# Kernel optimization log

Hardware: AMD Instinct MI355X
Metric: run time of the kernel (lower is better)

The kernel has to match this reference:

```python
import jax, jax.numpy as jnp
import numpy as np

N = 100000
E = 3200000
G = 64  # number of graphs


def _lin_params(key, fan_in, fan_out):
    k1, k2 = jax.random.split(key)
    bound = 1.0 / np.sqrt(fan_in)
    W = jax.random.uniform(k1, (fan_in, fan_out), jnp.float32, -bound, bound)
    b = jax.random.uniform(k2, (fan_out,), jnp.float32, -bound, bound)
    return W, b


def setup_inputs() -> dict:
    key = jax.random.key(0)
    ks = jax.random.split(key, 12)
    x = jax.random.normal(ks[0], (N, 3), jnp.float32)
    edge_index = jax.random.randint(ks[1], (2, E), 0, N, jnp.int32)
    batch = jnp.sort(jax.random.randint(ks[2], (N,), 0, G, jnp.int32))
    # conv1: in=3, heads=4, out_channels=16, concat=True -> 64
    Wq1, bq1 = _lin_params(ks[3], 3, 64)
    Wk1, bk1 = _lin_params(ks[4], 3, 64)
    Wv1, bv1 = _lin_params(ks[5], 3, 64)
    Ws1, bs1 = _lin_params(ks[6], 3, 64)
    # conv2: in=64, heads=1, out_channels=6, concat=False -> 6
    Wq2, bq2 = _lin_params(ks[7], 64, 6)
    Wk2, bk2 = _lin_params(ks[8], 64, 6)
    Wv2, bv2 = _lin_params(ks[9], 64, 6)
    Ws2, bs2 = _lin_params(ks[10], 64, 6)
    return dict(x=x, edge_index=edge_index, batch=batch,
                Wq1=Wq1, bq1=bq1, Wk1=Wk1, bk1=bk1, Wv1=Wv1, bv1=bv1, Ws1=Ws1, bs1=bs1,
                Wq2=Wq2, bq2=bq2, Wk2=Wk2, bk2=bk2, Wv2=Wv2, bv2=bv2, Ws2=Ws2, bs2=bs2)


def transformer_conv(x, src, dst, Wq, bq, Wk, bk, Wv, bv, Ws, bs, heads, d, concat):
    n = x.shape[0]
    q = (x @ Wq + bq).reshape(n, heads, d)
    k = (x @ Wk + bk).reshape(n, heads, d)
    v = (x @ Wv + bv).reshape(n, heads, d)
    # per-edge attention logits: query at target, key at source  [E, H]
    logits = jnp.einsum('ehd,ehd->eh', q[dst], k[src]) / jnp.sqrt(jnp.float32(d))
    # segment softmax over incoming edges of each target node
    m = jax.ops.segment_max(logits, dst, num_segments=n)          # [N, H]
    a = jnp.exp(logits - m[dst])                                   # [E, H]
    denom = jax.ops.segment_sum(a, dst, num_segments=n)           # [N, H]
    alpha = a / (denom[dst] + 1e-16)
    out = jax.ops.segment_sum(alpha[:, :, None] * v[src], dst, num_segments=n)  # [N,H,d]
    out = out.reshape(n, heads * d) if concat else out.mean(axis=1)
    return out + x @ Ws + bs  # root/skip connection


def reference(x, edge_index, batch,
              Wq1, bq1, Wk1, bk1, Wv1, bv1, Ws1, bs1,
              Wq2, bq2, Wk2, bk2, Wv2, bv2, Ws2, bs2):
    src, dst = edge_index[0], edge_index[1]
    h = transformer_conv(x, src, dst, Wq1, bq1, Wk1, bk1, Wv1, bv1, Ws1, bs1,
                         heads=4, d=16, concat=True)
    h = jax.nn.relu(h)
    # dropout is identity in eval mode
    h = transformer_conv(h, src, dst, Wq2, bq2, Wk2, bk2, Wv2, bv2, Ws2, bs2,
                         heads=1, d=6, concat=False)
    # global mean pool over graphs
    sums = jax.ops.segment_sum(h, batch, num_segments=G)
    cnts = jax.ops.segment_sum(jnp.ones((h.shape[0],), h.dtype), batch, num_segments=G)
    pooled = sums / jnp.maximum(cnts, 1.0)[:, None]
    return jax.nn.log_softmax(pooled, axis=1)
```

## Files before the change

### kernel.cpp

```cpp
#include <hip/hip_runtime.h>
#include <hip/hip_fp16.h>
#include <math.h>

#define N_NODES 100000
#define N_EDGES 3200000
#define N_GRAPHS 64
#define NEG_INF -1e30f

#define NB 196
#define CAP 18432
#define NBLK 512
#define CHUNK 6250

__device__ __forceinline__ void atomAddF(float* p, float v) {
#if defined(__HIP_PLATFORM_AMD__)
    unsafeAtomicAdd(p, v);
#else
    atomicAdd(p, v);
#endif
}

__device__ __forceinline__ float b2f(unsigned w, int sh) {
    return (float)(signed char)(w >> sh);
}

__device__ __forceinline__ float kvdot(const float* q, uint4 w, float* sv_out) {
    float2 s = __half22float2(*(const __half2*)&w.w);
    *sv_out = s.y;
    return s.x * (q[0] * b2f(w.x, 0) + q[1] * b2f(w.x, 8)
                + q[2] * b2f(w.x, 16) + q[3] * b2f(w.x, 24)
                + q[4] * b2f(w.y, 0) + q[5] * b2f(w.y, 8));
}

__global__ void k0_packx(const float* __restrict__ x, float4* __restrict__ xp,
                         uint2* __restrict__ xh) {
    int n = blockIdx.x * 256 + threadIdx.x;
    if (n >= N_NODES) return;
    float x0 = x[3 * n], x1 = x[3 * n + 1], x2 = x[3 * n + 2];
    xp[n] = make_float4(x0, x1, x2, 0.f);
    __half2 h01 = __floats2half2_rn(x0, x1);
    __half2 h2p = __floats2half2_rn(x2, 0.f);
    xh[n] = make_uint2(*(unsigned*)&h01, *(unsigned*)&h2p);
}

__global__ __launch_bounds__(512) void s1_partition(const int* __restrict__ ei,
                                                    int* __restrict__ offs,
                                                    unsigned* __restrict__ pairs) {
    __shared__ unsigned pairbuf[CHUNK];
    __shared__ unsigned sortbuf[CHUNK];
    __shared__ unsigned char buckbuf[CHUNK];
    __shared__ int hist[4][200];
    __shared__ int cur[NB], tmp[NB];
    int tid = threadIdx.x;
    int wp = tid >> 7;
    for (int i = tid; i < 4 * 200; i += 512) ((int*)hist)[i] = 0;
    __syncthreads();
    int gbase = blockIdx.x * CHUNK;
    for (int i = tid; i < CHUNK; i += 512) {
        int src = ei[gbase + i];
        unsigned dst = (unsigned)ei[N_EDGES + gbase + i];
        pairbuf[i] = ((unsigned)src << 9) | (dst & 511u);
        unsigned b = dst >> 9;
        buckbuf[i] = (unsigned char)b;
        atomicAdd(&hist[wp][b], 1);
    }
    __syncthreads();
    if (tid < NB)
        tmp[tid] = hist[0][tid] + hist[1][tid] + hist[2][tid] + hist[3][tid];
    __syncthreads();
    for (int off = 1; off < NB; off <<= 1) {
        int v = 0;
        if (tid < NB && tid >= off) v = tmp[tid - off];
        __syncthreads();
        if (tid < NB) tmp[tid] += v;
        __syncthreads();
    }
    if (tid < NB) {
        int cnt_b = hist[0][tid] + hist[1][tid] + hist[2][tid] + hist[3][tid];
        int excl = tmp[tid] - cnt_b;
        cur[tid] = excl;
        offs[blockIdx.x * NB + tid] = excl;
    }
    __syncthreads();
    for (int i = tid; i < CHUNK; i += 512) {
        int pos = atomicAdd(&cur[buckbuf[i]], 1);
        sortbuf[pos] = pairbuf[i];
    }
    __syncthreads();
    for (int i = tid; i < CHUNK; i += 512)
        pairs[gbase + i] = sortbuf[i];
}

#define B4T 1024
__global__ __launch_bounds__(B4T) void b4_build(const unsigned* __restrict__ pairs,
                                                const int* __restrict__ offs,
                                                int* __restrict__ rs,
                                                int* __restrict__ re,
                                                int* __restrict__ csr_src) {
    __shared__ unsigned eLDS[CAP];
    __shared__ int so[NBLK], slen[NBLK], dbase[NBLK];
    __shared__ int cnt[512], sc[512], cur[512];
    int b = blockIdx.x;
    int tid = threadIdx.x;

    for (int k = tid; k < NBLK; k += B4T) {
        int s = offs[k * NB + b];
        int e = (b == NB - 1) ? CHUNK : offs[k * NB + b + 1];
        so[k] = s;
        slen[k] = e - s;
    }
    __syncthreads();
    if (tid < NBLK) sc[tid] = slen[tid];
    __syncthreads();
    for (int off = 1; off < NBLK; off <<= 1) {
        int v = (tid < NBLK && tid >= off) ? sc[tid - off] : 0;
        __syncthreads();
        if (tid < NBLK) sc[tid] += v;
        __syncthreads();
    }
    if (tid < NBLK) dbase[tid] = sc[tid] - slen[tid];
    __syncthreads();
    int ne = dbase[NBLK - 1] + slen[NBLK - 1];

    int wave = tid >> 6, lane = tid & 63;
    for (int k = wave; k < NBLK; k += (B4T / 64)) {
        int gb = k * CHUNK + so[k];
        int db = dbase[k], ln = slen[k];
        for (int i = lane; i < ln; i += 64)
            eLDS[db + i] = pairs[gb + i];
    }
    if (tid < 512) cnt[tid] = 0;
    __syncthreads();

    for (int i = tid; i < ne; i += B4T)
        atomicAdd(&cnt[eLDS[i] & 511u], 1);
    __syncthreads();
    if (tid < 512) sc[tid] = cnt[tid];
    __syncthreads();
    for (int off = 1; off < 512; off <<= 1) {
        int v = (tid < 512 && tid >= off) ? sc[tid - off] : 0;
        __syncthreads();
        if (tid < 512) sc[tid] += v;
        __syncthreads();
    }
    int rbase = b * CAP;
    if (tid < 512) {
        int excl = sc[tid] - cnt[tid];
        cur[tid] = rbase + excl;
        int node = (b << 9) + tid;
        if (node < N_NODES) {
            rs[node] = rbase + excl;
            re[node] = rbase + sc[tid];
        }
    }
    __syncthreads();
    for (int i = tid; i < ne; i += B4T) {
        unsigned p = eLDS[i];
        int pos = atomicAdd(&cur[p & 511u], 1);
        csr_src[pos] = (int)(p >> 9);
    }
}

__global__ void g1_layer1(const float4* __restrict__ xp,
                          const uint2* __restrict__ xh,
                          const float* __restrict__ Wq, const float* __restrict__ bq,
                          const float* __restrict__ Wk, const float* __restrict__ bk,
                          const float* __restrict__ Wv, const float* __restrict__ bv,
                          const float* __restrict__ Ws, const float* __restrict__ bs,
                          const int* __restrict__ rs, const int* __restrict__ re,
                          const int* __restrict__ csr_src,
                          uint2* __restrict__ h1) {
    __shared__ float sWq[192], sWk[192], sWv[192], sWs[192];
    __shared__ float sbq[64], sbk[64], sbv[64], sbs[64];
    for (int i = threadIdx.x; i < 192; i += 256) {
        sWq[i] = Wq[i]; sWk[i] = Wk[i]; sWv[i] = Wv[i]; sWs[i] = Ws[i];
    }
    for (int i = threadIdx.x; i < 64; i += 256) {
        sbq[i] = bq[i]; sbk[i] = bk[i]; sbv[i] = bv[i]; sbs[i] = bs[i];
    }
    __syncthreads();

    int lane = threadIdx.x & 63;
    int u = lane & 15;
    int slot = u >> 2;
    int j0 = u * 4;
    int n = blockIdx.x * 16 + (threadIdx.x >> 6) * 4 + (lane >> 4);

    float4 xc = xp[n];
    float x0 = xc.x, x1 = xc.y, x2 = xc.z;

    float q[4];
#pragma unroll
    for (int i = 0; i < 4; ++i)
        q[i] = 0.25f * (sbq[j0 + i] + x0 * sWq[j0 + i] + x1 * sWq[64 + j0 + i]
                        + x2 * sWq[128 + j0 + i]);
    float t0 = 0.f, t1 = 0.f, t2 = 0.f, tb = 0.f;
#pragma unroll
    for (int i = 0; i < 4; ++i) {
        float qi = q[i];
        t0 += qi * sWk[j0 + i];
        t1 += qi * sWk[64 + j0 + i];
        t2 += qi * sWk[128 + j0 + i];
        tb += qi * sbk[j0 + i];
    }
#pragma unroll
    for (int off = 1; off <= 2; off <<= 1) {
        t0 += __shfl_xor(t0, off);
        t1 += __shfl_xor(t1, off);
        t2 += __shfl_xor(t2, off);
        tb += __shfl_xor(tb, off);
    }
    int tsrc = (lane & 48) | ((lane & 3) << 2) | ((lane >> 2) & 3);
    t0 = __shfl(t0, tsrc, 64);
    t1 = __shfl(t1, tsrc, 64);
    t2 = __shfl(t2, tsrc, 64);
    tb = __shfl(tb, tsrc, 64);

    int row = rs[n];
    int deg = re[n] - row;

    float mA = NEG_INF, dA = 0.f, s0A = 0.f, s1A = 0.f, s2A = 0.f;
    float mB = NEG_INF, dB = 0.f, s0B = 0.f, s1B = 0.f, s2B = 0.f;
    for (int base = 0; base < deg; base += 8) {
        int eA = base + slot, eB = base + 4 + slot;
        bool vA = eA < deg, vB = eB < deg;
        int srcA = vA ? csr_src[row + eA] : 0;
        int srcB = vB ? csr_src[row + eB] : 0;
        uint2 wA = xh[srcA];
        uint2 wB = xh[srcB];
        float2 a01 = __half22float2(*(const __half2*)&wA.x);
        float a2 = __half22float2(*(const __half2*)&wA.y).x;
        float2 b01 = __half22float2(*(const __half2*)&wB.x);
        float b2 = __half22float2(*(const __half2*)&wB.y).x;
        float lA = vA ? (tb + a01.x * t0 + a01.y * t1 + a2 * t2) : NEG_INF;
        float lB = vB ? (tb + b01.x * t0 + b01.y * t1 + b2 * t2) : NEG_INF;
        float mnA = fmaxf(mA, lA);
        float scA = __expf(mA - mnA);
        float aA = vA ? __expf(lA - mnA) : 0.f;
        dA = dA * scA + aA;
        s0A = s0A * scA + aA * a01.x;
        s1A = s1A * scA + aA * a01.y;
        s2A = s2A * scA + aA * a2;
        mA = mnA;
        float mnB = fmaxf(mB, lB);
        float scB = __expf(mB - mnB);
        float aB = vB ? __expf(lB - mnB) : 0.f;
        dB = dB * scB + aB;
        s0B = s0B * scB + aB * b01.x;
        s1B = s1B * scB + aB * b01.y;
        s2B = s2B * scB + aB * b2;
        mB = mnB;
    }
    float m = fmaxf(mA, mB);
    float fA = __expf(mA - m), fB = __expf(mB - m);
    float d = dA * fA + dB * fB;
    float s0 = s0A * fA + s0B * fB;
    float s1 = s1A * fA + s1B * fB;
    float s2 = s2A * fA + s2B * fB;

    float gm = m;
    gm = fmaxf(gm, __shfl_xor(gm, 4));
    gm = fmaxf(gm, __shfl_xor(gm, 8));
    float f = __expf(m - gm);
    d *= f; s0 *= f; s1 *= f; s2 *= f;
#pragma unroll
    for (int off = 4; off <= 8; off <<= 1) {
        d += __shfl_xor(d, off);
        s0 += __shfl_xor(s0, off);
        s1 += __shfl_xor(s1, off);
        s2 += __shfl_xor(s2, off);
    }

    int esrc = (lane & 48) | ((lane >> 2) & 3);
    float dH = __shfl(d, esrc, 64);
    float s0H = __shfl(s0, esrc, 64);
    float s1H = __shfl(s1, esrc, 64);
    float s2H = __shfl(s2, esrc, 64);
    float inv = 1.f / (dH + 1e-16f);
    float fr = dH * inv, r0 = s0H * inv, r1 = s1H * inv, r2 = s2H * inv;

    float o[4];
#pragma unroll
    for (int i = 0; i < 4; ++i) {
        int j = j0 + i;
        float val = fr * sbv[j] + r0 * sWv[j] + r1 * sWv[64 + j] + r2 * sWv[128 + j]
                  + sbs[j] + x0 * sWs[j] + x1 * sWs[64 + j] + x2 * sWs[128 + j];
        o[i] = fmaxf(val, 0.f);
    }
    __half2 p01 = __floats2half2_rn(o[0], o[1]);
    __half2 p23 = __floats2half2_rn(o[2], o[3]);
    h1[(size_t)n * 16 + u] = make_uint2(*(unsigned*)&p01, *(unsigned*)&p23);
}

__global__ void k5_node2(const unsigned* __restrict__ h1,
                         const float* __restrict__ Wq, const float* __restrict__ bq,
                         const float* __restrict__ Wk, const float* __restrict__ bk,
                         const float* __restrict__ Wv, const float* __restrict__ bv,
                         const float* __restrict__ Ws, const float* __restrict__ bs,
                         float* __restrict__ q2, float* __restrict__ s2,
                         uint4* __restrict__ kv2) {
    __shared__ float sWq[384], sWk[384], sWv[384], sWs[384];
    __shared__ float sbq[6], sbk[6], sbv[6], sbs[6];
    for (int i = threadIdx.x; i < 384; i += blockDim.x) {
        sWq[i] = Wq[i]; sWk[i] = Wk[i]; sWv[i] = Wv[i]; sWs[i] = Ws[i];
    }
    if (threadIdx.x < 6) {
        sbq[threadIdx.x] = bq[threadIdx.x];
        sbk[threadIdx.x] = bk[threadIdx.x];
        sbv[threadIdx.x] = bv[threadIdx.x];
        sbs[threadIdx.x] = bs[threadIdx.x];
    }
    __syncthreads();
    int n = blockIdx.x * blockDim.x + threadIdx.x;
    if (n >= N_NODES) return;
    float qa[6], ka[6], va[6], sa[6];
#pragma unroll
    for (int c = 0; c < 6; ++c) { qa[c] = sbq[c]; ka[c] = sbk[c]; va[c] = sbv[c]; sa[c] = sbs[c]; }
    const uint4* hp = reinterpret_cast<const uint4*>(h1 + (size_t)n * 32);
#pragma unroll
    for (int i4 = 0; i4 < 8; ++i4) {
        uint4 hv = hp[i4];
        float2 f01 = __half22float2(*(const __half2*)&hv.x);
        float2 f23 = __half22float2(*(const __half2*)&hv.y);
        float2 f45 = __half22float2(*(const __half2*)&hv.z);
        float2 f67 = __half22float2(*(const __half2*)&hv.w);
        float hvv[8] = {f01.x, f01.y, f23.x, f23.y, f45.x, f45.y, f67.x, f67.y};
#pragma unroll
        for (int uu = 0; uu < 8; ++uu) {
            float hx = hvv[uu];
            int i = i4 * 8 + uu;
#pragma unroll
            for (int c = 0; c < 6; ++c) {
                qa[c] += hx * sWq[i * 6 + c];
                ka[c] += hx * sWk[i * 6 + c];
                va[c] += hx * sWv[i * 6 + c];
                sa[c] += hx * sWs[i * 6 + c];
            }
        }
    }
    const float rsqrt6 = 0.4082482904638631f;
#pragma unroll
    for (int c = 0; c < 6; ++c) {
        q2[(size_t)n * 6 + c] = qa[c] * rsqrt6;
        s2[(size_t)n * 6 + c] = sa[c];
    }
    float mk = 0.f, mv = 0.f;
#pragma unroll
    for (int c = 0; c < 6; ++c) {
        mk = fmaxf(mk, fabsf(ka[c]));
        mv = fmaxf(mv, fabsf(va[c]));
    }
    float sk = fmaxf(mk, 1e-8f) * (1.f / 127.f);
    float sv = fmaxf(mv, 1e-8f) * (1.f / 127.f);
    float isk = 1.f / sk, isv = 1.f / sv;
    int qk[6], qv[6];
#pragma unroll
    for (int c = 0; c < 6; ++c) {
        qk[c] = __float2int_rn(ka[c] * isk);
        qv[c] = __float2int_rn(va[c] * isv);
    }
    uint4 w;
    w.x = (qk[0] & 255) | ((qk[1] & 255) << 8) | ((qk[2] & 255) << 16) | ((qk[3] & 255) << 24);
    w.y = (qk[4] & 255) | ((qk[5] & 255) << 8) | ((qv[0] & 255) << 16) | ((qv[1] & 255) << 24);
    w.z = (qv[2] & 255) | ((qv[3] & 255) << 8) | ((qv[4] & 255) << 16) | ((qv[5] & 255) << 24);
    __half2 hs = __floats2half2_rn(sk, sv);
    w.w = *(unsigned*)&hs;
    kv2[n] = w;
}

__global__ void g2_layer2(const int* __restrict__ rs, const int* __restrict__ re,
                          const int* __restrict__ csr_src,
                          const float* __restrict__ q2,
                          const uint4* __restrict__ kv2,
                          const float* __restrict__ s2,
                          const int* __restrict__ batch,
                          float* __restrict__ psum, float* __restrict__ pcnt) {
    __shared__ float bsum[N_GRAPHS * 6];
    __shared__ float bcnt[N_GRAPHS];
    for (int i = threadIdx.x; i < N_GRAPHS * 6; i += 256) bsum[i] = 0.f;
    for (int i = threadIdx.x; i < N_GRAPHS; i += 256) bcnt[i] = 0.f;
    __syncthreads();

    int node = blockIdx.x * 32 + (threadIdx.x >> 3);
    int lane8 = threadIdx.x & 7;

    float q[6];
#pragma unroll
    for (int c = 0; c < 6; ++c) q[c] = q2[(size_t)node * 6 + c];
    int row = rs[node];
    int deg = re[node] - row;

    float lg[8], svr[8];
    unsigned py[8], pz[8];
#pragma unroll
    for (int i = 0; i < 8; ++i) { lg[i] = NEG_INF; svr[i] = 0.f; py[i] = 0u; pz[i] = 0u; }
    float lmax = NEG_INF;
#pragma unroll
    for (int i = 0; i < 4; ++i) {
        int e = lane8 + i * 8;
        bool v = e < deg;
        int src = v ? csr_src[row + e] : 0;
        uint4 w = kv2[src];
        float svx;
        float l = kvdot(q, w, &svx);
        if (v) {
            lg[i] = l; svr[i] = svx; py[i] = w.y; pz[i] = w.z;
            lmax = fmaxf(lmax, l);
        }
    }
    if (deg > 32) {
#pragma unroll
        for (int i = 4; i < 8; ++i) {
            int e = lane8 + i * 8;
            bool v = e < deg;
            int src = v ? csr_src[row + e] : 0;
            uint4 w = kv2[src];
            float svx;
            float l = kvdot(q, w, &svx);
            if (v) {
                lg[i] = l; svr[i] = svx; py[i] = w.y; pz[i] = w.z;
                lmax = fmaxf(lmax, l);
            }
        }
    }
    float mo = NEG_INF, dov = 0.f;
    float ao[6] = {0.f, 0.f, 0.f, 0.f, 0.f, 0.f};
    for (int e = lane8 + 64; e < deg; e += 8) {
        int src = csr_src[row + e];
        uint4 w = kv2[src];
        float svx;
        float l = kvdot(q, w, &svx);
        float mn = fmaxf(mo, l);
        float scp = __expf(mo - mn);
        float wx = __expf(l - mn);
        float wsx = wx * svx;
        dov = dov * scp + wx;
        ao[0] = ao[0] * scp + wsx * b2f(w.y, 16);
        ao[1] = ao[1] * scp + wsx * b2f(w.y, 24);
        ao[2] = ao[2] * scp + wsx * b2f(w.z, 0);
        ao[3] = ao[3] * scp + wsx * b2f(w.z, 8);
        ao[4] = ao[4] * scp + wsx * b2f(w.z, 16);
        ao[5] = ao[5] * scp + wsx * b2f(w.z, 24);
        mo = mn;
    }
    lmax = fmaxf(lmax, mo);
    lmax = fmaxf(lmax, __shfl_xor(lmax, 1));
    lmax = fmaxf(lmax, __shfl_xor(lmax, 2));
    lmax = fmaxf(lmax, __shfl_xor(lmax, 4));
    if (lmax < -5e29f) lmax = 0.f;

    float d = 0.f;
    float acc[6] = {0.f, 0.f, 0.f, 0.f, 0.f, 0.f};
#pragma unroll
    for (int i = 0; i < 8; ++i) {
        float w = __expf(lg[i] - lmax);
        float ws = w * svr[i];
        d += w;
        acc[0] += ws * b2f(py[i], 16);
        acc[1] += ws * b2f(py[i], 24);
        acc[2] += ws * b2f(pz[i], 0);
        acc[3] += ws * b2f(pz[i], 8);
        acc[4] += ws * b2f(pz[i], 16);
        acc[5] += ws * b2f(pz[i], 24);
    }
    float so = __expf(mo - lmax);
    d += dov * so;
#pragma unroll
    for (int c = 0; c < 6; ++c) acc[c] += ao[c] * so;

#pragma unroll
    for (int off = 1; off <= 4; off <<= 1) {
        d += __shfl_xor(d, off);
#pragma unroll
        for (int c = 0; c < 6; ++c) acc[c] += __shfl_xor(acc[c], off);
    }

    if (lane8 == 0) {
        float inv = 1.f / (d + 1e-16f);
        int g = batch[node];
#pragma unroll
        for (int c = 0; c < 6; ++c) {
            float val = acc[c] * inv + s2[(size_t)node * 6 + c];
            atomicAdd(&bsum[g * 6 + c], val);
        }
        atomicAdd(&bcnt[g], 1.f);
    }
    __syncthreads();
    for (int i = threadIdx.x; i < N_GRAPHS * 6; i += 256) {
        float v = bsum[i];
        if (v != 0.f) atomAddF(psum + i, v);
    }
    for (int i = threadIdx.x; i < N_GRAPHS; i += 256) {
        float v = bcnt[i];
        if (v != 0.f) atomAddF(pcnt + i, v);
    }
}

__global__ void k9_final(const float* __restrict__ psum, const float* __restrict__ pcnt,
                         float* __restrict__ out) {
    int g = threadIdx.x;
    if (g >= N_GRAPHS) return;
    float cnt = fmaxf(pcnt[g], 1.0f);
    float z[6];
    float mx = -1e30f;
#pragma unroll
    for (int c = 0; c < 6; ++c) {
        z[c] = psum[g * 6 + c] / cnt;
        mx = fmaxf(mx, z[c]);
    }
    float se = 0.f;
#pragma unroll
    for (int c = 0; c < 6; ++c) se += __expf(z[c] - mx);
    float lse = mx + logf(se);
#pragma unroll
    for (int c = 0; c < 6; ++c) out[g * 6 + c] = z[c] - lse;
}

extern "C" void kernel_launch(void* const* d_in, const int* in_sizes, int n_in,
                              void* d_out, int out_size, void* d_ws, size_t ws_size,
                              hipStream_t stream) {
    const float* x   = (const float*)d_in[0];
    const int*   ei  = (const int*)d_in[1];
    const int*   bat = (const int*)d_in[2];
    const float* Wq1 = (const float*)d_in[3];  const float* bq1 = (const float*)d_in[4];
    const float* Wk1 = (const float*)d_in[5];  const float* bk1 = (const float*)d_in[6];
    const float* Wv1 = (const float*)d_in[7];  const float* bv1 = (const float*)d_in[8];
    const float* Ws1 = (const float*)d_in[9];  const float* bs1 = (const float*)d_in[10];
    const float* Wq2 = (const float*)d_in[11]; const float* bq2 = (const float*)d_in[12];
    const float* Wk2 = (const float*)d_in[13]; const float* bk2 = (const float*)d_in[14];
    const float* Wv2 = (const float*)d_in[15]; const float* bv2 = (const float*)d_in[16];
    const float* Ws2 = (const float*)d_in[17]; const float* bs2 = (const float*)d_in[18];
    float* out = (float*)d_out;

    char* ws = (char*)d_ws;
    size_t off = 0;
    auto alloc = [&](size_t bytes) -> char* {
        char* p = ws + off;
        off += (bytes + 255) & ~(size_t)255;
        return p;
    };

    float* psum = (float*)alloc((size_t)N_GRAPHS * 6 * 4);
    float* pcnt = (float*)alloc((size_t)N_GRAPHS * 4);
    size_t zero_bytes = off;

    int*      offs    = (int*)     alloc((size_t)NBLK * NB * 4);
    unsigned* pairs   = (unsigned*)alloc((size_t)N_EDGES * 4);
    int*      csr_src = (int*)     alloc((size_t)NB * CAP * 4);
    int*      rsv     = (int*)     alloc((size_t)N_NODES * 4);
    int*      rev     = (int*)     alloc((size_t)N_NODES * 4);
    float4*   xp      = (float4*)  alloc((size_t)N_NODES * 16);
    uint2*    xh      = (uint2*)   alloc((size_t)N_NODES * 8);
    unsigned* h1      = (unsigned*)alloc((size_t)N_NODES * 64 * 2);
    float*    q2      = (float*)   alloc((size_t)N_NODES * 6 * 4);
    float*    s2      = (float*)   alloc((size_t)N_NODES * 6 * 4);
    uint4*    kv2     = (uint4*)   alloc((size_t)N_NODES * 16);

    hipMemsetAsync(d_ws, 0, zero_bytes, stream);

    k0_packx<<<(N_NODES + 255) / 256, 256, 0, stream>>>(x, xp, xh);
    s1_partition<<<NBLK, 512, 0, stream>>>(ei, offs, pairs);
    b4_build<<<NB, B4T, 0, stream>>>(pairs, offs, rsv, rev, csr_src);

    g1_layer1<<<N_NODES / 16, 256, 0, stream>>>(xp, xh, Wq1, bq1, Wk1, bk1, Wv1, bv1,
                                                Ws1, bs1, rsv, rev, csr_src,
                                                (uint2*)h1);
    k5_node2<<<(N_NODES + 255) / 256, 256, 0, stream>>>(h1, Wq2, bq2, Wk2, bk2,
                                                        Wv2, bv2, Ws2, bs2,
                                                        q2, s2, kv2);
    g2_layer2<<<N_NODES / 32, 256, 0, stream>>>(rsv, rev, csr_src, q2, kv2, s2,
                                                bat, psum, pcnt);
    k9_final<<<1, 64, 0, stream>>>(psum, pcnt, out);
}
```

Measured before the change: 144.4 us.

## Fuse layer-2 node projections into layer-1 kernel and spread histogram atomics

Folds the second-layer Q/K/V/skip projections into the layer-1 aggregation kernel. Each lane computes partial dot products over its four output channels and the partials are reduced with cross-lane shuffles. This drops the h1 intermediate buffer (a 12.8MB write plus read) and one kernel launch. The query vector is now stored in fp16, which shrinks the g2 load but adds rounding error. Separately, the partition and CSR-build histograms use more privatised copies to reduce LDS atomic contention. The cost is extra shuffle work and more shared memory in g1.

Result: slower. 158.1 us (+9.5%).

```diff
diff --git a/kernel.cpp b/kernel.cpp
--- a/kernel.cpp
+++ b/kernel.cpp
@@ -49,11 +49,11 @@
     __shared__ unsigned pairbuf[CHUNK];
     __shared__ unsigned sortbuf[CHUNK];
     __shared__ unsigned char buckbuf[CHUNK];
-    __shared__ int hist[4][200];
+    __shared__ int hist[8][200];
     __shared__ int cur[NB], tmp[NB];
     int tid = threadIdx.x;
-    int wp = tid >> 7;
-    for (int i = tid; i < 4 * 200; i += 512) ((int*)hist)[i] = 0;
+    int wp = tid >> 6;
+    for (int i = tid; i < 8 * 200; i += 512) ((int*)hist)[i] = 0;
     __syncthreads();
     int gbase = blockIdx.x * CHUNK;
     for (int i = tid; i < CHUNK; i += 512) {
@@ -65,8 +65,13 @@
         atomicAdd(&hist[wp][b], 1);
     }
     __syncthreads();
-    if (tid < NB)
-        tmp[tid] = hist[0][tid] + hist[1][tid] + hist[2][tid] + hist[3][tid];
+    if (tid < NB) {
+        int s = 0;
+#pragma unroll
+        for (int w = 0; w < 8; ++w) s += hist[w][tid];
+        tmp[tid] = s;
+        hist[0][tid] = s;
+    }
     __syncthreads();
     for (int off = 1; off < NB; off <<= 1) {
         int v = 0;
@@ -76,8 +81,7 @@
         __syncthreads();
     }
     if (tid < NB) {
-        int cnt_b = hist[0][tid] + hist[1][tid] + hist[2][tid] + hist[3][tid];
-        int excl = tmp[tid] - cnt_b;
+        int excl = tmp[tid] - hist[0][tid];
         cur[tid] = excl;
         offs[blockIdx.x * NB + tid] = excl;
     }
@@ -99,7 +103,8 @@
                                                 int* __restrict__ csr_src) {
     __shared__ unsigned eLDS[CAP];
     __shared__ int so[NBLK], slen[NBLK], dbase[NBLK];
-    __shared__ int cnt[512], sc[512], cur[512];
+    __shared__ int cnt2[2][512];
+    __shared__ int sc[512], cur[512];
     int b = blockIdx.x;
     int tid = threadIdx.x;
 
@@ -109,6 +114,7 @@
         so[k] = s;
         slen[k] = e - s;
     }
+    ((int*)cnt2)[tid] = 0;
     __syncthreads();
     if (tid < NBLK) sc[tid] = slen[tid];
     __syncthreads();
@@ -129,13 +135,17 @@
         for (int i = lane; i < ln; i += 64)
             eLDS[db + i] = pairs[gb + i];
     }
-    if (tid < 512) cnt[tid] = 0;
-    __syncthreads();
-
+    __syncthreads();
+
+    int half = tid >> 9;
     for (int i = tid; i < ne; i += B4T)
-        atomicAdd(&cnt[eLDS[i] & 511u], 1);
-    __syncthreads();
-    if (tid < 512) sc[tid] = cnt[tid];
+        atomicAdd(&cnt2[half][eLDS[i] & 511u], 1);
+    __syncthreads();
+    int mycnt = 0;
+    if (tid < 512) {
+        mycnt = cnt2[0][tid] + cnt2[1][tid];
+        sc[tid] = mycnt;
+    }
     __syncthreads();
     for (int off = 1; off < 512; off <<= 1) {
         int v = (tid < 512 && tid >= off) ? sc[tid - off] : 0;
@@ -145,7 +155,7 @@
     }
     int rbase = b * CAP;
     if (tid < 512) {
-        int excl = sc[tid] - cnt[tid];
+        int excl = sc[tid] - mycnt;
         cur[tid] = rbase + excl;
         int node = (b << 9) + tid;
         if (node < N_NODES) {
@@ -161,22 +171,38 @@
     }
 }
 
-__global__ void g1_layer1(const float4* __restrict__ xp,
-                          const uint2* __restrict__ xh,
-                          const float* __restrict__ Wq, const float* __restrict__ bq,
-                          const float* __restrict__ Wk, const float* __restrict__ bk,
-                          const float* __restrict__ Wv, const float* __restrict__ bv,
-                          const float* __restrict__ Ws, const float* __restrict__ bs,
-                          const int* __restrict__ rs, const int* __restrict__ re,
-                          const int* __restrict__ csr_src,
-                          uint2* __restrict__ h1) {
+__global__ void g1_fused(const float4* __restrict__ xp,
+                         const uint2* __restrict__ xh,
+                         const float* __restrict__ Wq, const float* __restrict__ bq,
+                         const float* __restrict__ Wk, const float* __restrict__ bk,
+                         const float* __restrict__ Wv, const float* __restrict__ bv,
+                         const float* __restrict__ Ws, const float* __restrict__ bs,
+                         const float* __restrict__ Wq2, const float* __restrict__ bq2,
+                         const float* __restrict__ Wk2, const float* __restrict__ bk2,
+                         const float* __restrict__ Wv2, const float* __restrict__ bv2,
+                         const float* __restrict__ Ws2, const float* __restrict__ bs2,
+                         const int* __restrict__ rs, const int* __restrict__ re,
+                         const int* __restrict__ csr_src,
+                         uint4* __restrict__ q2h, float* __restrict__ s2,
+                         uint4* __restrict__ kv2) {
     __shared__ float sWq[192], sWk[192], sWv[192], sWs[192];
     __shared__ float sbq[64], sbk[64], sbv[64], sbs[64];
+    __shared__ float sW2q[384], sW2k[384], sW2v[384], sW2s[384];
+    __shared__ float sb2q[6], sb2k[6], sb2v[6], sb2s[6];
     for (int i = threadIdx.x; i < 192; i += 256) {
         sWq[i] = Wq[i]; sWk[i] = Wk[i]; sWv[i] = Wv[i]; sWs[i] = Ws[i];
     }
     for (int i = threadIdx.x; i < 64; i += 256) {
         sbq[i] = bq[i]; sbk[i] = bk[i]; sbv[i] = bv[i]; sbs[i] = bs[i];
+    }
+    for (int i = threadIdx.x; i < 384; i += 256) {
+        sW2q[i] = Wq2[i]; sW2k[i] = Wk2[i]; sW2v[i] = Wv2[i]; sW2s[i] = Ws2[i];
+    }
+    if (threadIdx.x < 6) {
+        sb2q[threadIdx.x] = bq2[threadIdx.x];
+        sb2k[threadIdx.x] = bk2[threadIdx.x];
+        sb2v[threadIdx.x] = bv2[threadIdx.x];
+        sb2s[threadIdx.x] = bs2[threadIdx.x];
     }
     __syncthreads();
 
@@ -256,26 +282,26 @@
     float d = dA * fA + dB * fB;
     float s0 = s0A * fA + s0B * fB;
     float s1 = s1A * fA + s1B * fB;
-    float s2 = s2A * fA + s2B * fB;
+    float s2v = s2A * fA + s2B * fB;
 
     float gm = m;
     gm = fmaxf(gm, __shfl_xor(gm, 4));
     gm = fmaxf(gm, __shfl_xor(gm, 8));
     float f = __expf(m - gm);
-    d *= f; s0 *= f; s1 *= f; s2 *= f;
+    d *= f; s0 *= f; s1 *= f; s2v *= f;
 #pragma unroll
     for (int off = 4; off <= 8; off <<= 1) {
         d += __shfl_xor(d, off);
         s0 += __shfl_xor(s0, off);
         s1 += __shfl_xor(s1, off);
-        s2 += __shfl_xor(s2, off);
+        s2v += __shfl_xor(s2v, off);
     }
 
     int esrc = (lane & 48) | ((lane >> 2) & 3);
     float dH = __shfl(d, esrc, 64);
     float s0H = __shfl(s0, esrc, 64);
     float s1H = __shfl(s1, esrc, 64);
-    float s2H = __shfl(s2, esrc, 64);
+    float s2H = __shfl(s2v, esrc, 64);
     float inv = 1.f / (dH + 1e-16f);
     float fr = dH * inv, r0 = s0H * inv, r1 = s1H * inv, r2 = s2H * inv;
 
@@ -287,90 +313,77 @@
                   + sbs[j] + x0 * sWs[j] + x1 * sWs[64 + j] + x2 * sWs[128 + j];
         o[i] = fmaxf(val, 0.f);
     }
-    __half2 p01 = __floats2half2_rn(o[0], o[1]);
-    __half2 p23 = __floats2half2_rn(o[2], o[3]);
-    h1[(size_t)n * 16 + u] = make_uint2(*(unsigned*)&p01, *(unsigned*)&p23);
-}
-
-__global__ void k5_node2(const unsigned* __restrict__ h1,
-                         const float* __restrict__ Wq, const float* __restrict__ bq,
-                         const float* __restrict__ Wk, const float* __restrict__ bk,
-                         const float* __restrict__ Wv, const float* __restrict__ bv,
-                         const float* __restrict__ Ws, const float* __restrict__ bs,
-                         float* __restrict__ q2, float* __restrict__ s2,
-                         uint4* __restrict__ kv2) {
-    __shared__ float sWq[384], sWk[384], sWv[384], sWs[384];
-    __shared__ float sbq[6], sbk[6], sbv[6], sbs[6];
-    for (int i = threadIdx.x; i < 384; i += blockDim.x) {
-        sWq[i] = Wq[i]; sWk[i] = Wk[i]; sWv[i] = Wv[i]; sWs[i] = Ws[i];
-    }
-    if (threadIdx.x < 6) {
-        sbq[threadIdx.x] = bq[threadIdx.x];
-        sbk[threadIdx.x] = bk[threadIdx.x];
-        sbv[threadIdx.x] = bv[threadIdx.x];
-        sbs[threadIdx.x] = bs[threadIdx.x];
-    }
-    __syncthreads();
-    int n = blockIdx.x * blockDim.x + threadIdx.x;
-    if (n >= N_NODES) return;
-    float qa[6], ka[6], va[6], sa[6];
-#pragma unroll
-    for (int c = 0; c < 6; ++c) { qa[c] = sbq[c]; ka[c] = sbk[c]; va[c] = sbv[c]; sa[c] = sbs[c]; }
-    const uint4* hp = reinterpret_cast<const uint4*>(h1 + (size_t)n * 32);
-#pragma unroll
-    for (int i4 = 0; i4 < 8; ++i4) {
-        uint4 hv = hp[i4];
-        float2 f01 = __half22float2(*(const __half2*)&hv.x);
-        float2 f23 = __half22float2(*(const __half2*)&hv.y);
-        float2 f45 = __half22float2(*(const __half2*)&hv.z);
-        float2 f67 = __half22float2(*(const __half2*)&hv.w);
-        float hvv[8] = {f01.x, f01.y, f23.x, f23.y, f45.x, f45.y, f67.x, f67.y};
-#pragma unroll
-        for (int uu = 0; uu < 8; ++uu) {
-            float hx = hvv[uu];
-            int i = i4 * 8 + uu;
-#pragma unroll
-            for (int c = 0; c < 6; ++c) {
-                qa[c] += hx * sWq[i * 6 + c];
-                ka[c] += hx * sWk[i * 6 + c];
-                va[c] += hx * sWv[i * 6 + c];
-                sa[c] += hx * sWs[i * 6 + c];
-            }
-        }
-    }
+
+    float pq[6], pk[6], pv[6], ps[6];
+#pragma unroll
+    for (int c = 0; c < 6; ++c) { pq[c] = 0.f; pk[c] = 0.f; pv[c] = 0.f; ps[c] = 0.f; }
+#pragma unroll
+    for (int i = 0; i < 4; ++i) {
+        float hx = o[i];
+        int jb = (j0 + i) * 6;
+#pragma unroll
+        for (int c = 0; c < 6; ++c) {
+            pq[c] += hx * sW2q[jb + c];
+            pk[c] += hx * sW2k[jb + c];
+            pv[c] += hx * sW2v[jb + c];
+            ps[c] += hx * sW2s[jb + c];
+        }
+    }
+#pragma unroll
+    for (int off = 1; off <= 8; off <<= 1) {
+#pragma unroll
+        for (int c = 0; c < 6; ++c) {
+            pq[c] += __shfl_xor(pq[c], off);
+            pk[c] += __shfl_xor(pk[c], off);
+            pv[c] += __shfl_xor(pv[c], off);
+            ps[c] += __shfl_xor(ps[c], off);
+        }
+    }
+
     const float rsqrt6 = 0.4082482904638631f;
-#pragma unroll
-    for (int c = 0; c < 6; ++c) {
-        q2[(size_t)n * 6 + c] = qa[c] * rsqrt6;
-        s2[(size_t)n * 6 + c] = sa[c];
-    }
-    float mk = 0.f, mv = 0.f;
-#pragma unroll
-    for (int c = 0; c < 6; ++c) {
-        mk = fmaxf(mk, fabsf(ka[c]));
-        mv = fmaxf(mv, fabsf(va[c]));
-    }
-    float sk = fmaxf(mk, 1e-8f) * (1.f / 127.f);
-    float sv = fmaxf(mv, 1e-8f) * (1.f / 127.f);
-    float isk = 1.f / sk, isv = 1.f / sv;
-    int qk[6], qv[6];
-#pragma unroll
-    for (int c = 0; c < 6; ++c) {
-        qk[c] = __float2int_rn(ka[c] * isk);
-        qv[c] = __float2int_rn(va[c] * isv);
-    }
-    uint4 w;
-    w.x = (qk[0] & 255) | ((qk[1] & 255) << 8) | ((qk[2] & 255) << 16) | ((qk[3] & 255) << 24);
-    w.y = (qk[4] & 255) | ((qk[5] & 255) << 8) | ((qv[0] & 255) << 16) | ((qv[1] & 255) << 24);
-    w.z = (qv[2] & 255) | ((qv[3] & 255) << 8) | ((qv[4] & 255) << 16) | ((qv[5] & 255) << 24);
-    __half2 hs = __floats2half2_rn(sk, sv);
-    w.w = *(unsigned*)&hs;
-    kv2[n] = w;
+    if (u == 0) {
+        __half2 h01 = __floats2half2_rn((pq[0] + sb2q[0]) * rsqrt6, (pq[1] + sb2q[1]) * rsqrt6);
+        __half2 h23 = __floats2half2_rn((pq[2] + sb2q[2]) * rsqrt6, (pq[3] + sb2q[3]) * rsqrt6);
+        __half2 h45 = __floats2half2_rn((pq[4] + sb2q[4]) * rsqrt6, (pq[5] + sb2q[5]) * rsqrt6);
+        uint4 w;
+        w.x = *(unsigned*)&h01; w.y = *(unsigned*)&h23;
+        w.z = *(unsigned*)&h45; w.w = 0u;
+        q2h[n] = w;
+    } else if (u == 1) {
+#pragma unroll
+        for (int c = 0; c < 6; ++c) s2[(size_t)n * 6 + c] = ps[c] + sb2s[c];
+    } else if (u == 2) {
+        float ka[6], va[6];
+#pragma unroll
+        for (int c = 0; c < 6; ++c) { ka[c] = pk[c] + sb2k[c]; va[c] = pv[c] + sb2v[c]; }
+        float mk = 0.f, mv = 0.f;
+#pragma unroll
+        for (int c = 0; c < 6; ++c) {
+            mk = fmaxf(mk, fabsf(ka[c]));
+            mv = fmaxf(mv, fabsf(va[c]));
+        }
+        float sk = fmaxf(mk, 1e-8f) * (1.f / 127.f);
+        float sv = fmaxf(mv, 1e-8f) * (1.f / 127.f);
+        float isk = 1.f / sk, isv = 1.f / sv;
+        int qk[6], qv[6];
+#pragma unroll
+        for (int c = 0; c < 6; ++c) {
+            qk[c] = __float2int_rn(ka[c] * isk);
+            qv[c] = __float2int_rn(va[c] * isv);
+        }
+        uint4 w;
+        w.x = (qk[0] & 255) | ((qk[1] & 255) << 8) | ((qk[2] & 255) << 16) | ((qk[3] & 255) << 24);
+        w.y = (qk[4] & 255) | ((qk[5] & 255) << 8) | ((qv[0] & 255) << 16) | ((qv[1] & 255) << 24);
+        w.z = (qv[2] & 255) | ((qv[3] & 255) << 8) | ((qv[4] & 255) << 16) | ((qv[5] & 255) << 24);
+        __half2 hs = __floats2half2_rn(sk, sv);
+        w.w = *(unsigned*)&hs;
+        kv2[n] = w;
+    }
 }
 
 __global__ void g2_layer2(const int* __restrict__ rs, const int* __restrict__ re,
                           const int* __restrict__ csr_src,
-                          const float* __restrict__ q2,
+                          const uint4* __restrict__ q2h,
                           const uint4* __restrict__ kv2,
                           const float* __restrict__ s2,
                           const int* __restrict__ batch,
@@ -384,9 +397,11 @@
     int node = blockIdx.x * 32 + (threadIdx.x >> 3);
     int lane8 = threadIdx.x & 7;
 
-    float q[6];
-#pragma unroll
-    for (int c = 0; c < 6; ++c) q[c] = q2[(size_t)node * 6 + c];
+    uint4 qw = q2h[node];
+    float2 q01 = __half22float2(*(const __half2*)&qw.x);
+    float2 q23 = __half22float2(*(const __half2*)&qw.y);
+    float2 q45 = __half22float2(*(const __half2*)&qw.z);
+    float q[6] = {q01.x, q01.y, q23.x, q23.y, q45.x, q45.y};
     int row = rs[node];
     int deg = re[node] - row;
 
@@ -551,8 +566,7 @@
     int*      rev     = (int*)     alloc((size_t)N_NODES * 4);
     float4*   xp      = (float4*)  alloc((size_t)N_NODES * 16);
     uint2*    xh      = (uint2*)   alloc((size_t)N_NODES * 8);
-    unsigned* h1      = (unsigned*)alloc((size_t)N_NODES * 64 * 2);
-    float*    q2      = (float*)   alloc((size_t)N_NODES * 6 * 4);
+    uint4*    q2h     = (uint4*)   alloc((size_t)N_NODES * 16);
     float*    s2      = (float*)   alloc((size_t)N_NODES * 6 * 4);
     uint4*    kv2     = (uint4*)   alloc((size_t)N_NODES * 16);
 
@@ -562,13 +576,11 @@
     s1_partition<<<NBLK, 512, 0, stream>>>(ei, offs, pairs);
     b4_build<<<NB, B4T, 0, stream>>>(pairs, offs, rsv, rev, csr_src);
 
-    g1_layer1<<<N_NODES / 16, 256, 0, stream>>>(xp, xh, Wq1, bq1, Wk1, bk1, Wv1, bv1,
-                                                Ws1, bs1, rsv, rev, csr_src,
-                                                (uint2*)h1);
-    k5_node2<<<(N_NODES + 255) / 256, 256, 0, stream>>>(h1, Wq2, bq2, Wk2, bk2,
-                                                        Wv2, bv2, Ws2, bs2,
-                                                        q2, s2, kv2);
-    g2_layer2<<<N_NODES / 32, 256, 0, stream>>>(rsv, rev, csr_src, q2, kv2, s2,
+    g1_fused<<<N_NODES / 16, 256, 0, stream>>>(xp, xh, Wq1, bq1, Wk1, bk1, Wv1, bv1,
+                                               Ws1, bs1, Wq2, bq2, Wk2, bk2,
+                                               Wv2, bv2, Ws2, bs2,
+                                               rsv, rev, csr_src, q2h, s2, kv2);
+    g2_layer2<<<N_NODES / 32, 256, 0, stream>>>(rsv, rev, csr_src, q2h, kv2, s2,
                                                 bat, psum, pcnt);
     k9_final<<<1, 64, 0, stream>>>(psum, pcnt, out);
 }
```
